# Kernel tuning notes

Measured on AMD Instinct MI355X. Metric: run time of the kernel, lower is better.

The kernel has to match this reference:

```python
import jax, jax.numpy as jnp
import numpy as np

CUTOFF = 32
NBINS = 2 * CUTOFF + 1  # 65 relative-position bins
LN_EPS = 1e-5


def setup_inputs() -> dict:
    key = jax.random.key(0)
    ks = jax.random.split(key, 9)
    N, D, H, SIZE = 1024, 256, 32, 64
    local = jax.random.normal(ks[0], (N, D), jnp.float32)
    resi = jnp.arange(N, dtype=jnp.int32)
    chain = jnp.sort(jax.random.randint(ks[1], (N,), 0, 2)).astype(jnp.int32)
    batch = jnp.sort(jax.random.randint(ks[2], (N,), 0, 2)).astype(jnp.int32)
    mask = jax.random.bernoulli(ks[3], 0.9, (N,))
    W_left = jax.random.normal(ks[4], (D, H), jnp.float32) / np.float32(np.sqrt(D))
    W_right = jax.random.normal(ks[5], (D, H), jnp.float32) / np.float32(np.sqrt(D))
    W_relpos = jax.random.normal(ks[6], (NBINS, H), jnp.float32) / np.float32(np.sqrt(NBINS))
    ln_scale = jnp.ones((H,), jnp.float32)
    ln_offset = jnp.zeros((H,), jnp.float32)
    W_hidden = jax.random.normal(ks[7], (H, H), jnp.float32) / np.float32(np.sqrt(H))
    W_out = jax.random.normal(ks[8], (H, SIZE), jnp.float32) / np.float32(np.sqrt(H))
    return dict(local=local, resi=resi, chain=chain, batch=batch, mask=mask,
                W_left=W_left, W_right=W_right, W_relpos=W_relpos,
                ln_scale=ln_scale, ln_offset=ln_offset,
                W_hidden=W_hidden, W_out=W_out)


def _layernorm(x, scale, offset):
    mu = x.mean(-1, keepdims=True)
    var = ((x - mu) ** 2).mean(-1, keepdims=True)
    return (x - mu) * jax.lax.rsqrt(var + LN_EPS) * scale + offset


def reference(local, resi, chain, batch, mask,
              W_left, W_right, W_relpos, ln_scale, ln_offset, W_hidden, W_out):
    # pairwise outer-sum of two linear projections: [N, N, 32]
    left = local @ W_left
    right = local @ W_right
    pair = left[:, None, :] + right[None, :, :]

    same_batch = batch[:, None] == batch[None, :]
    same_chain = (chain[:, None] == chain[None, :]) & same_batch
    # clipped relative position -> one_hot @ W_relpos == gather of W_relpos rows
    diff = jnp.clip(resi[:, None] - resi[None, :], -CUTOFF, CUTOFF) + CUTOFF
    rel = jnp.where(same_chain[..., None], W_relpos[diff], 0.0)
    pair = pair + rel

    pair = _layernorm(pair, ln_scale, ln_offset)

    # 2-layer GELU MLP, no bias
    hidden = jax.nn.gelu(pair @ W_hidden)
    result = hidden @ W_out

    pair_mask = (mask[:, None] & mask[None, :]) & same_batch
    return jnp.where(pair_mask[..., None], result, 0.0)
```

## Files before the change

### kernel.cpp

```cpp
#include <hip/hip_runtime.h>

#define NN 1024
#define DD 256
#define HH 32
#define SS 64

typedef short bf16x8 __attribute__((ext_vector_type(8)));
typedef float f32x4  __attribute__((ext_vector_type(4)));

__device__ __forceinline__ unsigned short f2bf(float f) {
    union { float f; unsigned int i; } v; v.f = f;
    unsigned int r = v.i + 0x7FFFu + ((v.i >> 16) & 1u);
    return (unsigned short)(r >> 16);
}

__device__ __forceinline__ float gelu_f(float x) {
    const float c1 = 0.7978845608028654f, c2 = 0.044715f;
    float u = c1 * fmaf(c2 * x * x, x, x);
    float e = __expf(-2.0f * fabsf(u));
    float th = (1.0f - e) / (1.0f + e);
    th = copysignf(th, u);
    return 0.5f * x * (1.0f + th);
}

__global__ __launch_bounds__(64) void proj_kernel(
    const float* __restrict__ local_,
    const float* __restrict__ Wl,
    const float* __restrict__ Wr,
    float* __restrict__ leftF, float* __restrict__ rightF)
{
    __shared__ float row[DD];
    const int i = blockIdx.x, t = threadIdx.x;
    float4 v = ((const float4*)(local_ + (size_t)i * DD))[t];
    row[4*t+0] = v.x; row[4*t+1] = v.y; row[4*t+2] = v.z; row[4*t+3] = v.w;
    __syncthreads();
    const int h = t & 31;
    const float* W = (t < 32) ? Wl : Wr;
    float acc = 0.0f;
    #pragma unroll 8
    for (int d = 0; d < DD; ++d) acc = fmaf(row[d], W[d*HH + h], acc);
    float* dst = (t < 32) ? leftF : rightF;
    dst[i*HH + h] = acc;
}

__global__ __launch_bounds__(256) void pair_kernel(
    const float* __restrict__ leftF, const float* __restrict__ rightF,
    const int* __restrict__ resi, const int* __restrict__ chain,
    const int* __restrict__ batch, const int* __restrict__ mask,
    const float* __restrict__ Wrel,
    const float* __restrict__ lnS, const float* __restrict__ lnO,
    const float* __restrict__ Wh, const float* __restrict__ Wout,
    float* __restrict__ out)
{
    __shared__ float relL[65 * 36];
    __shared__ unsigned short WhT[32 * 32];
    __shared__ unsigned short WoT[64 * 32];
    __shared__ unsigned short hidL[4 * 16 * 40];

    const int tid  = threadIdx.x;
    const int wave = tid >> 6;
    const int lane = tid & 63;
    const int q    = lane >> 4;
    const int p    = lane & 15;
    const int i    = blockIdx.y;
    const int jb   = blockIdx.x;

    for (int idx = tid; idx < 65 * 32; idx += 256)
        relL[(idx >> 5) * 36 + (idx & 31)] = Wrel[idx];
    for (int idx = tid; idx < 32 * 32; idx += 256) {
        int k = idx >> 5, n = idx & 31;
        WhT[n * 32 + k] = f2bf(Wh[idx]);
    }
    for (int idx = tid; idx < 64 * 32; idx += 256) {
        int k = idx >> 6, s = idx & 63;
        WoT[s * 32 + k] = f2bf(Wout[idx]);
    }
    __syncthreads();

    const int bi = batch[i], ci = chain[i], ri = resi[i], mi = mask[i];
    float left8[8], lnS8[8], lnO8[8];
    {
        const float4 l0 = *(const float4*)&leftF[i * HH + 8 * q];
        const float4 l1 = *(const float4*)&leftF[i * HH + 8 * q + 4];
        left8[0]=l0.x; left8[1]=l0.y; left8[2]=l0.z; left8[3]=l0.w;
        left8[4]=l1.x; left8[5]=l1.y; left8[6]=l1.z; left8[7]=l1.w;
        #pragma unroll
        for (int e = 0; e < 8; ++e) { lnS8[e] = lnS[8*q + e]; lnO8[e] = lnO[8*q + e]; }
    }
    const bf16x8 whB0 = *(const bf16x8*)&WhT[(p      ) * 32 + 8 * q];
    const bf16x8 whB1 = *(const bf16x8*)&WhT[(16 + p ) * 32 + 8 * q];
    bf16x8 woB[4];
    #pragma unroll
    for (int t = 0; t < 4; ++t)
        woB[t] = *(const bf16x8*)&WoT[(16 * t + p) * 32 + 8 * q];

    unsigned short* hidw = &hidL[wave * 16 * 40];

    for (int it = 0; it < 4; ++it) {
        const int jbase = jb * 256 + it * 64 + wave * 16;
        const int j = jbase + p;

        const int bj = batch[j], cj = chain[j], rj = resi[j], mj = mask[j];
        const bool sb = (bi == bj);
        const bool sc = sb && (ci == cj);
        const float pm = (sb && (mi != 0) && (mj != 0)) ? 1.0f : 0.0f;

        float pr[8];
        {
            const float4 r0 = *(const float4*)&rightF[(size_t)j * HH + 8 * q];
            const float4 r1 = *(const float4*)&rightF[(size_t)j * HH + 8 * q + 4];
            pr[0]=left8[0]+r0.x; pr[1]=left8[1]+r0.y; pr[2]=left8[2]+r0.z; pr[3]=left8[3]+r0.w;
            pr[4]=left8[4]+r1.x; pr[5]=left8[5]+r1.y; pr[6]=left8[6]+r1.z; pr[7]=left8[7]+r1.w;
        }
        if (sc) {
            int d = ri - rj; d = d < -32 ? -32 : (d > 32 ? 32 : d);
            const float4 e0 = *(const float4*)&relL[(d + 32) * 36 + 8 * q];
            const float4 e1 = *(const float4*)&relL[(d + 32) * 36 + 8 * q + 4];
            pr[0]+=e0.x; pr[1]+=e0.y; pr[2]+=e0.z; pr[3]+=e0.w;
            pr[4]+=e1.x; pr[5]+=e1.y; pr[6]+=e1.z; pr[7]+=e1.w;
        }

        float s = 0.0f;
        #pragma unroll
        for (int e = 0; e < 8; ++e) s += pr[e];
        s += __shfl_xor(s, 16, 64);
        s += __shfl_xor(s, 32, 64);
        const float mu = s * (1.0f / HH);
        float v = 0.0f;
        #pragma unroll
        for (int e = 0; e < 8; ++e) { float dd = pr[e] - mu; v = fmaf(dd, dd, v); }
        v += __shfl_xor(v, 16, 64);
        v += __shfl_xor(v, 32, 64);
        const float rs = rsqrtf(v * (1.0f / HH) + 1e-5f);

        bf16x8 aF;
        #pragma unroll
        for (int e = 0; e < 8; ++e)
            aF[e] = (short)f2bf(fmaf((pr[e] - mu) * rs, lnS8[e], lnO8[e]));

        f32x4 z = {0.f, 0.f, 0.f, 0.f};
        f32x4 h0 = __builtin_amdgcn_mfma_f32_16x16x32_bf16(aF, whB0, z, 0, 0, 0);
        f32x4 h1 = __builtin_amdgcn_mfma_f32_16x16x32_bf16(aF, whB1, z, 0, 0, 0);

        #pragma unroll
        for (int r = 0; r < 4; ++r) {
            const int pr_row = 4 * q + r;
            hidw[pr_row * 40 + p]      = f2bf(gelu_f(h0[r]));
            hidw[pr_row * 40 + p + 16] = f2bf(gelu_f(h1[r]));
        }
        __syncthreads();
        const bf16x8 aH = *(const bf16x8*)&hidw[p * 40 + 8 * q];

        f32x4 o0 = __builtin_amdgcn_mfma_f32_16x16x32_bf16(aH, woB[0], z, 0, 0, 0);
        f32x4 o1 = __builtin_amdgcn_mfma_f32_16x16x32_bf16(aH, woB[1], z, 0, 0, 0);
        f32x4 o2 = __builtin_amdgcn_mfma_f32_16x16x32_bf16(aH, woB[2], z, 0, 0, 0);
        f32x4 o3 = __builtin_amdgcn_mfma_f32_16x16x32_bf16(aH, woB[3], z, 0, 0, 0);

        float pmv[4];
        #pragma unroll
        for (int r = 0; r < 4; ++r) pmv[r] = __shfl(pm, 4 * q + r, 64);

        #pragma unroll
        for (int r = 0; r < 4; ++r) {
            float* orow = out + ((size_t)i * NN + (size_t)(jbase + 4 * q + r)) * SS + p;
            orow[ 0] = o0[r] * pmv[r];
            orow[16] = o1[r] * pmv[r];
            orow[32] = o2[r] * pmv[r];
            orow[48] = o3[r] * pmv[r];
        }
        __syncthreads();
    }
}

extern "C" void kernel_launch(void* const* d_in, const int* in_sizes, int n_in,
                              void* d_out, int out_size, void* d_ws, size_t ws_size,
                              hipStream_t stream)
{
    const float* local_ = (const float*)d_in[0];
    const int* resi  = (const int*)d_in[1];
    const int* chain = (const int*)d_in[2];
    const int* batch = (const int*)d_in[3];
    const int* mask  = (const int*)d_in[4];
    const float* Wl   = (const float*)d_in[5];
    const float* Wr   = (const float*)d_in[6];
    const float* Wrel = (const float*)d_in[7];
    const float* lnS  = (const float*)d_in[8];
    const float* lnO  = (const float*)d_in[9];
    const float* Wh   = (const float*)d_in[10];
    const float* Wout = (const float*)d_in[11];
    float* out = (float*)d_out;

    float* leftF  = (float*)d_ws;
    float* rightF = leftF + NN * HH;

    proj_kernel<<<dim3(NN), dim3(64), 0, stream>>>(local_, Wl, Wr, leftF, rightF);
    pair_kernel<<<dim3(4, NN), dim3(256), 0, stream>>>(
        leftF, rightF, resi, chain, batch, mask, Wrel, lnS, lnO, Wh, Wout, out);
}
```

Measured before the change: 311.0 us.

## Drop block barriers, prefetch next j-tile, pack hidden LDS stores

Each wave uses its own LDS slice for the hidden tile, so both per-iteration block-wide __syncthreads are removed and waves run the loop independently. The next iteration's rightF rows and batch/chain/resi/mask values are loaded one iteration ahead to hide global latency. Hidden GELU outputs are written as packed 32-bit pairs with an interleaved K order, and the Wout transpose is permuted to match. Correctness now relies on intra-wave lockstep ordering of the LDS writes and reads. The prefetched registers add some register pressure.

```diff
diff --git a/kernel.cpp b/kernel.cpp
--- a/kernel.cpp
+++ b/kernel.cpp
@@ -72,8 +72,9 @@
         WhT[n * 32 + k] = f2bf(Wh[idx]);
     }
     for (int idx = tid; idx < 64 * 32; idx += 256) {
-        int k = idx >> 6, s = idx & 63;
-        WoT[s * 32 + k] = f2bf(Wout[idx]);
+        int k2 = idx >> 6, s = idx & 63;
+        int k  = (k2 >> 1) + (k2 & 1) * 16;
+        WoT[s * 32 + k2] = f2bf(Wout[k * SS + s]);
     }
     __syncthreads();
 
@@ -96,24 +97,33 @@
 
     unsigned short* hidw = &hidL[wave * 16 * 40];
 
+    const int j00 = jb * 256 + wave * 16;
+    float4 ra = *(const float4*)&rightF[(size_t)(j00 + p) * HH + 8 * q];
+    float4 rb = *(const float4*)&rightF[(size_t)(j00 + p) * HH + 8 * q + 4];
+    int bj = batch[j00 + p], cj = chain[j00 + p], rj = resi[j00 + p], mj = mask[j00 + p];
+
+    #pragma unroll 1
     for (int it = 0; it < 4; ++it) {
-        const int jbase = jb * 256 + it * 64 + wave * 16;
-        const int j = jbase + p;
-
-        const int bj = batch[j], cj = chain[j], rj = resi[j], mj = mask[j];
-        const bool sb = (bi == bj);
-        const bool sc = sb && (ci == cj);
-        const float pm = (sb && (mi != 0) && (mj != 0)) ? 1.0f : 0.0f;
+        const float4 cra = ra, crb = rb;
+        const int cbj = bj, ccj = cj, crj = rj, cmj = mj;
+        const int jbase = j00 + it * 64;
+
+        if (it < 3) {
+            const int nj = jbase + 64 + p;
+            ra = *(const float4*)&rightF[(size_t)nj * HH + 8 * q];
+            rb = *(const float4*)&rightF[(size_t)nj * HH + 8 * q + 4];
+            bj = batch[nj]; cj = chain[nj]; rj = resi[nj]; mj = mask[nj];
+        }
+
+        const bool sb = (bi == cbj);
+        const bool sc = sb && (ci == ccj);
+        const float pm = (sb && (mi != 0) && (cmj != 0)) ? 1.0f : 0.0f;
 
         float pr[8];
-        {
-            const float4 r0 = *(const float4*)&rightF[(size_t)j * HH + 8 * q];
-            const float4 r1 = *(const float4*)&rightF[(size_t)j * HH + 8 * q + 4];
-            pr[0]=left8[0]+r0.x; pr[1]=left8[1]+r0.y; pr[2]=left8[2]+r0.z; pr[3]=left8[3]+r0.w;
-            pr[4]=left8[4]+r1.x; pr[5]=left8[5]+r1.y; pr[6]=left8[6]+r1.z; pr[7]=left8[7]+r1.w;
-        }
+        pr[0]=left8[0]+cra.x; pr[1]=left8[1]+cra.y; pr[2]=left8[2]+cra.z; pr[3]=left8[3]+cra.w;
+        pr[4]=left8[4]+crb.x; pr[5]=left8[5]+crb.y; pr[6]=left8[6]+crb.z; pr[7]=left8[7]+crb.w;
         if (sc) {
-            int d = ri - rj; d = d < -32 ? -32 : (d > 32 ? 32 : d);
+            int d = ri - crj; d = d < -32 ? -32 : (d > 32 ? 32 : d);
             const float4 e0 = *(const float4*)&relL[(d + 32) * 36 + 8 * q];
             const float4 e1 = *(const float4*)&relL[(d + 32) * 36 + 8 * q + 4];
             pr[0]+=e0.x; pr[1]+=e0.y; pr[2]+=e0.z; pr[3]+=e0.w;
@@ -145,10 +155,10 @@
         #pragma unroll
         for (int r = 0; r < 4; ++r) {
             const int pr_row = 4 * q + r;
-            hidw[pr_row * 40 + p]      = f2bf(gelu_f(h0[r]));
-            hidw[pr_row * 40 + p + 16] = f2bf(gelu_f(h1[r]));
-        }
-        __syncthreads();
+            unsigned int pk = (unsigned int)f2bf(gelu_f(h0[r]))
+                            | ((unsigned int)f2bf(gelu_f(h1[r])) << 16);
+            *(unsigned int*)&hidw[pr_row * 40 + 2 * p] = pk;
+        }
         const bf16x8 aH = *(const bf16x8*)&hidw[p * 40 + 8 * q];
 
         f32x4 o0 = __builtin_amdgcn_mfma_f32_16x16x32_bf16(aH, woB[0], z, 0, 0, 0);
@@ -168,7 +178,6 @@
             orow[32] = o2[r] * pmv[r];
             orow[48] = o3[r] * pmv[r];
         }
-        __syncthreads();
     }
 }
 
```

Measured after the change: 312.6 us. About the same (+0.5%).
